# Kernel optimization log

Hardware: AMD Instinct MI355X
Metric: run time of the kernel (lower is better)

## Reference

```python
import jax, jax.numpy as jnp
from jax import lax
import numpy as np

POOL = 9   # nms_threshold*2 + 1
PAD = 4    # POOL // 2


def setup_inputs() -> dict:
    key = jax.random.key(0)
    x = jax.random.normal(key, (4, 256, 200, 320), dtype=jnp.float32)
    return {"x": x}


def reference(x):
    # x: [B, C, H, W]
    depth_wise_max = jnp.max(x, axis=1, keepdims=True)          # [B,1,H,W]
    is_depth_wise_max = x == depth_wise_max                      # [B,C,H,W] bool
    # 9x9 local max pool, stride 1, pad 4 (torch pads with -inf for max_pool2d)
    local_max = lax.reduce_window(
        x, -jnp.inf, lax.max,
        window_dimensions=(1, 1, POOL, POOL),
        window_strides=(1, 1, 1, 1),
        padding=[(0, 0), (0, 0), (PAD, PAD), (PAD, PAD)],
    )
    is_local_max = x == local_max
    prob = jnp.where(is_depth_wise_max & is_local_max, x, jnp.zeros((), x.dtype)).sum(axis=1)  # [B,H,W]
    return prob
```

## Files before the change

kernel.cpp:

```cpp
#include <hip/hip_runtime.h>
#include <math.h>

#define B_   4
#define C_   256
#define H_   200
#define W_   320
#define HW   (H_ * W_)
#define BHW  (B_ * HW)

#define TH   50
#define TW   64
#define PR   58
#define PCW  72
#define PSTRIDE 76
#define HSTRIDE 68
#define CS   16
#define CPG  (C_ / CS)

static_assert(TH * 4 == H_, "H tiling");
static_assert(TW * 5 == W_, "W tiling");

__device__ __forceinline__ void win9(const float v[16], float w[8]) {
  float m1[15];
#pragma unroll
  for (int i = 0; i < 15; ++i) m1[i] = fmaxf(v[i], v[i + 1]);
  float m2[13];
#pragma unroll
  for (int i = 0; i < 13; ++i) m2[i] = fmaxf(m1[i], m1[i + 2]);
  float m4[9];
#pragma unroll
  for (int i = 0; i < 9; ++i)  m4[i] = fmaxf(m2[i], m2[i + 4]);
#pragma unroll
  for (int i = 0; i < 8; ++i)  w[i] = fmaxf(m4[i], v[i + 8]);
}

__global__ __launch_bounds__(256) void hdm_main(const float* __restrict__ x,
                                                float* __restrict__ wsM,
                                                float* __restrict__ wsP) {
  __shared__ float patch[PR * PSTRIDE];
  __shared__ float hmax[PR * HSTRIDE];

  const int tile = blockIdx.x;
  const int b    = blockIdx.y;
  const int cg   = blockIdx.z;
  const int th   = tile / 5, tw = tile % 5;
  const int h0 = th * TH, w0 = tw * TW;
  const int tid = (int)threadIdx.x;

  const int rvA   = tid;
  const int rsegA = rvA >> 6, cwA = rvA & 63;
  const int r0A   = rsegA * 8;
  const int rvB   = tid + 256;
  const bool actB = rvB < 7 * 64;
  const int rsegB = rvB >> 6, cwB = rvB & 63;
  const int r0B   = rsegB * 8;
  const int kvB   = (rsegB == 6) ? 2 : 8;

  float accM0[8], accP0[8], accM1[8], accP1[8];
#pragma unroll
  for (int i = 0; i < 8; ++i) {
    accM0[i] = -INFINITY; accP0[i] = 0.f;
    accM1[i] = -INFINITY; accP1[i] = 0.f;
  }

  for (int cc = 0; cc < CPG; ++cc) {
    const int c = cg * CPG + cc;
    const float* xp = x + (size_t)(b * C_ + c) * HW;

    for (int q = tid; q < PR * 18; q += 256) {
      const int pr = q / 18, c4 = q % 18;
      const int pc = c4 * 4;
      const int gh = h0 - 4 + pr;
      const int gw = w0 - 4 + pc;
      float4 v;
      if (gh < 0 || gh >= H_) {
        v.x = v.y = v.z = v.w = -INFINITY;
      } else if (gw >= 0 && gw + 3 < W_) {
        v = *reinterpret_cast<const float4*>(xp + (size_t)gh * W_ + gw);
      } else {
        const float* row = xp + (size_t)gh * W_;
        v.x = (gw + 0 >= 0 && gw + 0 < W_) ? row[gw + 0] : -INFINITY;
        v.y = (gw + 1 >= 0 && gw + 1 < W_) ? row[gw + 1] : -INFINITY;
        v.z = (gw + 2 >= 0 && gw + 2 < W_) ? row[gw + 2] : -INFINITY;
        v.w = (gw + 3 >= 0 && gw + 3 < W_) ? row[gw + 3] : -INFINITY;
      }
      *reinterpret_cast<float4*>(&patch[pr * PSTRIDE + pc]) = v;
    }
    __syncthreads();

    for (int rr = tid; rr < PR * 8; rr += 256) {
      const int r = rr >> 3, seg = rr & 7;
      const float* prow = &patch[r * PSTRIDE + seg * 8];
      const float4 a0 = *reinterpret_cast<const float4*>(prow + 0);
      const float4 a1 = *reinterpret_cast<const float4*>(prow + 4);
      const float4 a2 = *reinterpret_cast<const float4*>(prow + 8);
      const float4 a3 = *reinterpret_cast<const float4*>(prow + 12);
      const float v[16] = {a0.x, a0.y, a0.z, a0.w, a1.x, a1.y, a1.z, a1.w,
                           a2.x, a2.y, a2.z, a2.w, a3.x, a3.y, a3.z, a3.w};
      float w[8];
      win9(v, w);
      float* hrow = &hmax[r * HSTRIDE + seg * 8];
      *reinterpret_cast<float4*>(hrow + 0) = make_float4(w[0], w[1], w[2], w[3]);
      *reinterpret_cast<float4*>(hrow + 4) = make_float4(w[4], w[5], w[6], w[7]);
    }
    __syncthreads();

    {
      float hv[16];
#pragma unroll
      for (int i = 0; i < 16; ++i) hv[i] = hmax[(r0A + i) * HSTRIDE + cwA];
      float w9v[8];
      win9(hv, w9v);
#pragma unroll
      for (int i = 0; i < 8; ++i) {
        const float xc  = patch[(r0A + 4 + i) * PSTRIDE + (cwA + 4)];
        const float add = (xc == w9v[i]) ? xc : 0.f;
        const bool  gt  = xc > accM0[i];
        const bool  eq  = xc == accM0[i];
        accP0[i] = gt ? add : (accP0[i] + (eq ? add : 0.f));
        accM0[i] = gt ? xc : accM0[i];
      }
    }
    if (actB) {
      float hv[16];
#pragma unroll
      for (int i = 0; i < 16; ++i) {
        int r = r0B + i;
        r = (r < PR) ? r : (PR - 1);
        hv[i] = hmax[r * HSTRIDE + cwB];
      }
      float w9v[8];
      win9(hv, w9v);
#pragma unroll
      for (int i = 0; i < 8; ++i) {
        if (i < kvB) {
          const float xc  = patch[(r0B + 4 + i) * PSTRIDE + (cwB + 4)];
          const float add = (xc == w9v[i]) ? xc : 0.f;
          const bool  gt  = xc > accM1[i];
          const bool  eq  = xc == accM1[i];
          accP1[i] = gt ? add : (accP1[i] + (eq ? add : 0.f));
          accM1[i] = gt ? xc : accM1[i];
        }
      }
    }
    __syncthreads();
  }

  const size_t obase = (size_t)cg * BHW + (size_t)b * HW;
#pragma unroll
  for (int i = 0; i < 8; ++i) {
    const int h = h0 + r0A + i, w = w0 + cwA;
    const size_t idx = obase + (size_t)h * W_ + w;
    wsM[idx] = accM0[i];
    wsP[idx] = accP0[i];
  }
  if (actB) {
#pragma unroll
    for (int i = 0; i < 8; ++i) {
      if (i < kvB) {
        const int h = h0 + r0B + i, w = w0 + cwB;
        const size_t idx = obase + (size_t)h * W_ + w;
        wsM[idx] = accM1[i];
        wsP[idx] = accP1[i];
      }
    }
  }
}

__global__ __launch_bounds__(256) void hdm_combine(const float* __restrict__ wsM,
                                                   const float* __restrict__ wsP,
                                                   float* __restrict__ out) {
  const int px = blockIdx.x * 256 + (int)threadIdx.x;
  if (px >= BHW) return;
  float gm = -INFINITY, p = 0.f;
#pragma unroll
  for (int cs = 0; cs < CS; ++cs) {
    const float m = wsM[(size_t)cs * BHW + px];
    const float q = wsP[(size_t)cs * BHW + px];
    const bool gt = m > gm;
    const bool eq = m == gm;
    p  = gt ? q : (p + (eq ? q : 0.f));
    gm = gt ? m : gm;
  }
  out[px] = p;
}

extern "C" void kernel_launch(void* const* d_in, const int* in_sizes, int n_in,
                              void* d_out, int out_size, void* d_ws, size_t ws_size,
                              hipStream_t stream) {
  const float* x = (const float*)d_in[0];
  float* wsM = (float*)d_ws;
  float* wsP = wsM + (size_t)CS * BHW;
  float* out = (float*)d_out;

  hipLaunchKernelGGL(hdm_main, dim3(20, B_, CS), dim3(256), 0, stream, x, wsM, wsP);
  hipLaunchKernelGGL(hdm_combine, dim3((BHW + 255) / 256), dim3(256), 0, stream,
                     wsM, wsP, out);
}
```

Before: 433.4 us.

## Load patch rows into registers with prefetch, compute horizontal max before LDS

Each thread now loads its 16-wide row segment straight from global memory into registers, computes the horizontal 9-wide max there, and writes only the hmax row and the center values to shared memory. This removes the staging patch buffer and one pass through shared memory. The next channel's loads are issued before the barrier so global latency overlaps with the current channel's compute. The window max now uses max3 chains, and launch bounds request 4 blocks per SM. In exchange, register pressure rises from the prefetched float4s, and edge handling now relies on clamped loads plus register shifts.

```diff
diff --git a/kernel.cpp b/kernel.cpp
--- a/kernel.cpp
+++ b/kernel.cpp
@@ -11,50 +11,69 @@
 #define TH   50
 #define TW   64
 #define PR   58
-#define PCW  72
-#define PSTRIDE 76
-#define HSTRIDE 68
+#define HSTR 68
+#define XSTR 68
 #define CS   16
 #define CPG  (C_ / CS)
 
 static_assert(TH * 4 == H_, "H tiling");
 static_assert(TW * 5 == W_, "W tiling");
 
-__device__ __forceinline__ void win9(const float v[16], float w[8]) {
-  float m1[15];
-#pragma unroll
-  for (int i = 0; i < 15; ++i) m1[i] = fmaxf(v[i], v[i + 1]);
-  float m2[13];
-#pragma unroll
-  for (int i = 0; i < 13; ++i) m2[i] = fmaxf(m1[i], m1[i + 2]);
-  float m4[9];
-#pragma unroll
-  for (int i = 0; i < 9; ++i)  m4[i] = fmaxf(m2[i], m2[i + 4]);
-#pragma unroll
-  for (int i = 0; i < 8; ++i)  w[i] = fmaxf(m4[i], v[i + 8]);
-}
-
-__global__ __launch_bounds__(256) void hdm_main(const float* __restrict__ x,
-                                                float* __restrict__ wsM,
-                                                float* __restrict__ wsP) {
-  __shared__ float patch[PR * PSTRIDE];
-  __shared__ float hmax[PR * HSTRIDE];
+__device__ __forceinline__ float max3f(float a, float b, float c) {
+  return fmaxf(fmaxf(a, b), c);
+}
+
+__device__ __forceinline__ void win9m3(const float v[16], float w[8]) {
+  float m3[14];
+#pragma unroll
+  for (int i = 0; i < 14; ++i) m3[i] = max3f(v[i], v[i + 1], v[i + 2]);
+#pragma unroll
+  for (int i = 0; i < 8; ++i)  w[i] = max3f(m3[i], m3[i + 3], m3[i + 6]);
+}
+
+#define LD4(p, o) (*reinterpret_cast<const float4*>((p) + (o)))
+
+__global__ __launch_bounds__(256, 4) void hdm_main(const float* __restrict__ x,
+                                                   float* __restrict__ wsM,
+                                                   float* __restrict__ wsP) {
+  __shared__ float hmax[PR * HSTR];
+  __shared__ float xcen[TH * XSTR];
 
   const int tile = blockIdx.x;
   const int b    = blockIdx.y;
   const int cg   = blockIdx.z;
-  const int th   = tile / 5, tw = tile % 5;
+  const int th = tile / 5, tw = tile % 5;
   const int h0 = th * TH, w0 = tw * TW;
   const int tid = (int)threadIdx.x;
 
-  const int rvA   = tid;
-  const int rsegA = rvA >> 6, cwA = rvA & 63;
-  const int r0A   = rsegA * 8;
-  const int rvB   = tid + 256;
-  const bool actB = rvB < 7 * 64;
-  const int rsegB = rvB >> 6, cwB = rvB & 63;
-  const int r0B   = rsegB * 8;
-  const int kvB   = (rsegB == 6) ? 2 : 8;
+  const float* xg = x + (size_t)(b * C_ + cg * CPG) * HW;
+
+  const int  rA   = tid >> 3, sA = tid & 7;
+  const int  ghA  = h0 - 4 + rA;
+  const bool rokA = (ghA >= 0) && (ghA < H_);
+  const int  gwA  = w0 - 4 + sA * 8;
+  const bool lftA = (gwA < 0), rgtA = (gwA + 16 > W_);
+  const int  gwcA = lftA ? 0 : (rgtA ? (W_ - 16) : gwA);
+  const int  ghcA = min(max(ghA, 0), H_ - 1);
+  const float* pA = xg + (size_t)ghcA * W_ + gwcA;
+  const bool wxA  = rokA && (rA >= 4) && (rA <= 53);
+
+  const bool actB1 = tid < (PR * 8 - 256);
+  const int  qB   = tid + 256;
+  const int  rB   = qB >> 3, sB = qB & 7;
+  const int  ghB  = h0 - 4 + rB;
+  const bool rokB = (ghB >= 0) && (ghB < H_);
+  const int  gwB  = w0 - 4 + sB * 8;
+  const bool lftB = (gwB < 0), rgtB = (gwB + 16 > W_);
+  const int  gwcB = lftB ? 0 : (rgtB ? (W_ - 16) : gwB);
+  const int  ghcB = min(max(ghB, 0), H_ - 1);
+  const float* pB = xg + (size_t)ghcB * W_ + gwcB;
+  const bool wxB  = rokB && (rB >= 4) && (rB <= 53);
+
+  const int rs2A = tid >> 6, cw2 = tid & 63, r02A = rs2A * 8;
+  const bool actB2 = tid < 192;
+  const int rs2B = (tid + 256) >> 6, r02B = rs2B * 8;
+  const int kvB2 = (rs2B == 6) ? 2 : 8;
 
   float accM0[8], accP0[8], accM1[8], accP1[8];
 #pragma unroll
@@ -63,79 +82,135 @@
     accM1[i] = -INFINITY; accP1[i] = 0.f;
   }
 
+  float4 A0 = LD4(pA, 0), A1 = LD4(pA, 4), A2 = LD4(pA, 8), A3 = LD4(pA, 12);
+  float4 B0, B1, B2, B3;
+  if (actB1) { B0 = LD4(pB, 0); B1 = LD4(pB, 4); B2 = LD4(pB, 8); B3 = LD4(pB, 12); }
+  pA += HW; pB += HW;
+
   for (int cc = 0; cc < CPG; ++cc) {
-    const int c = cg * CPG + cc;
-    const float* xp = x + (size_t)(b * C_ + c) * HW;
-
-    for (int q = tid; q < PR * 18; q += 256) {
-      const int pr = q / 18, c4 = q % 18;
-      const int pc = c4 * 4;
-      const int gh = h0 - 4 + pr;
-      const int gw = w0 - 4 + pc;
-      float4 v;
-      if (gh < 0 || gh >= H_) {
-        v.x = v.y = v.z = v.w = -INFINITY;
-      } else if (gw >= 0 && gw + 3 < W_) {
-        v = *reinterpret_cast<const float4*>(xp + (size_t)gh * W_ + gw);
-      } else {
-        const float* row = xp + (size_t)gh * W_;
-        v.x = (gw + 0 >= 0 && gw + 0 < W_) ? row[gw + 0] : -INFINITY;
-        v.y = (gw + 1 >= 0 && gw + 1 < W_) ? row[gw + 1] : -INFINITY;
-        v.z = (gw + 2 >= 0 && gw + 2 < W_) ? row[gw + 2] : -INFINITY;
-        v.w = (gw + 3 >= 0 && gw + 3 < W_) ? row[gw + 3] : -INFINITY;
-      }
-      *reinterpret_cast<float4*>(&patch[pr * PSTRIDE + pc]) = v;
-    }
+    float wA[8];
+    float4 xAlo, xAhi;
+    {
+      const float t[16] = {A0.x, A0.y, A0.z, A0.w, A1.x, A1.y, A1.z, A1.w,
+                           A2.x, A2.y, A2.z, A2.w, A3.x, A3.y, A3.z, A3.w};
+      float v[16];
+      if (lftA) {
+#pragma unroll
+        for (int j = 0; j < 4;  ++j) v[j] = -INFINITY;
+#pragma unroll
+        for (int j = 4; j < 16; ++j) v[j] = t[j - 4];
+      } else if (rgtA) {
+#pragma unroll
+        for (int j = 0; j < 12; ++j) v[j] = t[j + 4];
+#pragma unroll
+        for (int j = 12; j < 16; ++j) v[j] = -INFINITY;
+      } else {
+#pragma unroll
+        for (int j = 0; j < 16; ++j) v[j] = t[j];
+      }
+      if (rokA) {
+        win9m3(v, wA);
+      } else {
+#pragma unroll
+        for (int i = 0; i < 8; ++i) wA[i] = -INFINITY;
+      }
+      xAlo = make_float4(v[4], v[5], v[6], v[7]);
+      xAhi = make_float4(v[8], v[9], v[10], v[11]);
+    }
+    float wB[8];
+    float4 xBlo, xBhi;
+    if (actB1) {
+      const float t[16] = {B0.x, B0.y, B0.z, B0.w, B1.x, B1.y, B1.z, B1.w,
+                           B2.x, B2.y, B2.z, B2.w, B3.x, B3.y, B3.z, B3.w};
+      float v[16];
+      if (lftB) {
+#pragma unroll
+        for (int j = 0; j < 4;  ++j) v[j] = -INFINITY;
+#pragma unroll
+        for (int j = 4; j < 16; ++j) v[j] = t[j - 4];
+      } else if (rgtB) {
+#pragma unroll
+        for (int j = 0; j < 12; ++j) v[j] = t[j + 4];
+#pragma unroll
+        for (int j = 12; j < 16; ++j) v[j] = -INFINITY;
+      } else {
+#pragma unroll
+        for (int j = 0; j < 16; ++j) v[j] = t[j];
+      }
+      if (rokB) {
+        win9m3(v, wB);
+      } else {
+#pragma unroll
+        for (int i = 0; i < 8; ++i) wB[i] = -INFINITY;
+      }
+      xBlo = make_float4(v[4], v[5], v[6], v[7]);
+      xBhi = make_float4(v[8], v[9], v[10], v[11]);
+    }
+
+    if (cc + 1 < CPG) {
+      A0 = LD4(pA, 0); A1 = LD4(pA, 4); A2 = LD4(pA, 8); A3 = LD4(pA, 12);
+      pA += HW;
+      if (actB1) {
+        B0 = LD4(pB, 0); B1 = LD4(pB, 4); B2 = LD4(pB, 8); B3 = LD4(pB, 12);
+        pB += HW;
+      }
+    }
+
     __syncthreads();
 
-    for (int rr = tid; rr < PR * 8; rr += 256) {
-      const int r = rr >> 3, seg = rr & 7;
-      const float* prow = &patch[r * PSTRIDE + seg * 8];
-      const float4 a0 = *reinterpret_cast<const float4*>(prow + 0);
-      const float4 a1 = *reinterpret_cast<const float4*>(prow + 4);
-      const float4 a2 = *reinterpret_cast<const float4*>(prow + 8);
-      const float4 a3 = *reinterpret_cast<const float4*>(prow + 12);
-      const float v[16] = {a0.x, a0.y, a0.z, a0.w, a1.x, a1.y, a1.z, a1.w,
-                           a2.x, a2.y, a2.z, a2.w, a3.x, a3.y, a3.z, a3.w};
-      float w[8];
-      win9(v, w);
-      float* hrow = &hmax[r * HSTRIDE + seg * 8];
-      *reinterpret_cast<float4*>(hrow + 0) = make_float4(w[0], w[1], w[2], w[3]);
-      *reinterpret_cast<float4*>(hrow + 4) = make_float4(w[4], w[5], w[6], w[7]);
-    }
+    {
+      float* hr = &hmax[rA * HSTR + sA * 8];
+      *reinterpret_cast<float4*>(hr + 0) = make_float4(wA[0], wA[1], wA[2], wA[3]);
+      *reinterpret_cast<float4*>(hr + 4) = make_float4(wA[4], wA[5], wA[6], wA[7]);
+      if (wxA) {
+        float* xr = &xcen[(rA - 4) * XSTR + sA * 8];
+        *reinterpret_cast<float4*>(xr + 0) = xAlo;
+        *reinterpret_cast<float4*>(xr + 4) = xAhi;
+      }
+      if (actB1) {
+        float* hrb = &hmax[rB * HSTR + sB * 8];
+        *reinterpret_cast<float4*>(hrb + 0) = make_float4(wB[0], wB[1], wB[2], wB[3]);
+        *reinterpret_cast<float4*>(hrb + 4) = make_float4(wB[4], wB[5], wB[6], wB[7]);
+        if (wxB) {
+          float* xrb = &xcen[(rB - 4) * XSTR + sB * 8];
+          *reinterpret_cast<float4*>(xrb + 0) = xBlo;
+          *reinterpret_cast<float4*>(xrb + 4) = xBhi;
+        }
+      }
+    }
+
     __syncthreads();
 
     {
       float hv[16];
 #pragma unroll
-      for (int i = 0; i < 16; ++i) hv[i] = hmax[(r0A + i) * HSTRIDE + cwA];
-      float w9v[8];
-      win9(hv, w9v);
+      for (int i = 0; i < 16; ++i) hv[i] = hmax[(r02A + i) * HSTR + cw2];
+      float w9[8];
+      win9m3(hv, w9);
 #pragma unroll
       for (int i = 0; i < 8; ++i) {
-        const float xc  = patch[(r0A + 4 + i) * PSTRIDE + (cwA + 4)];
-        const float add = (xc == w9v[i]) ? xc : 0.f;
+        const float xc  = xcen[(r02A + i) * XSTR + cw2];
+        const float add = (xc == w9[i]) ? xc : 0.f;
         const bool  gt  = xc > accM0[i];
         const bool  eq  = xc == accM0[i];
         accP0[i] = gt ? add : (accP0[i] + (eq ? add : 0.f));
         accM0[i] = gt ? xc : accM0[i];
       }
     }
-    if (actB) {
+    if (actB2) {
       float hv[16];
 #pragma unroll
       for (int i = 0; i < 16; ++i) {
-        int r = r0B + i;
-        r = (r < PR) ? r : (PR - 1);
-        hv[i] = hmax[r * HSTRIDE + cwB];
-      }
-      float w9v[8];
-      win9(hv, w9v);
+        const int r = min(r02B + i, PR - 1);
+        hv[i] = hmax[r * HSTR + cw2];
+      }
+      float w9[8];
+      win9m3(hv, w9);
 #pragma unroll
       for (int i = 0; i < 8; ++i) {
-        if (i < kvB) {
-          const float xc  = patch[(r0B + 4 + i) * PSTRIDE + (cwB + 4)];
-          const float add = (xc == w9v[i]) ? xc : 0.f;
+        if (i < kvB2) {
+          const float xc  = xcen[(r02B + i) * XSTR + cw2];
+          const float add = (xc == w9[i]) ? xc : 0.f;
           const bool  gt  = xc > accM1[i];
           const bool  eq  = xc == accM1[i];
           accP1[i] = gt ? add : (accP1[i] + (eq ? add : 0.f));
@@ -149,17 +224,15 @@
   const size_t obase = (size_t)cg * BHW + (size_t)b * HW;
 #pragma unroll
   for (int i = 0; i < 8; ++i) {
-    const int h = h0 + r0A + i, w = w0 + cwA;
-    const size_t idx = obase + (size_t)h * W_ + w;
+    const size_t idx = obase + (size_t)(h0 + r02A + i) * W_ + (w0 + cw2);
     wsM[idx] = accM0[i];
     wsP[idx] = accP0[i];
   }
-  if (actB) {
+  if (actB2) {
 #pragma unroll
     for (int i = 0; i < 8; ++i) {
-      if (i < kvB) {
-        const int h = h0 + r0B + i, w = w0 + cwB;
-        const size_t idx = obase + (size_t)h * W_ + w;
+      if (i < kvB2) {
+        const size_t idx = obase + (size_t)(h0 + r02B + i) * W_ + (w0 + cw2);
         wsM[idx] = accM1[i];
         wsP[idx] = accP1[i];
       }
```

Result: slower. 551.7 us (+27.3%).

## Load rows directly to registers, double-buffer LDS, and cut barriers per channel

Applied to the files above, without the earlier changes.

Each thread now loads its 16-wide row segment straight from global memory into registers and computes the horizontal 9-max in registers. This removes the raw patch staging in shared memory, and the next channel's loads are prefetched while the current one is processed. The hmax and centre buffers are double-buffered so each channel needs a single __syncthreads instead of three. The block grows to 512 threads with one output column-group per thread, and the window max uses max3 chains. Edge handling relies on shifting clamped loads, and register pressure from the prefetch may limit occupancy.

```diff
diff --git a/kernel.cpp b/kernel.cpp
--- a/kernel.cpp
+++ b/kernel.cpp
@@ -11,157 +11,143 @@
 #define TH   50
 #define TW   64
 #define PR   58
-#define PCW  72
-#define PSTRIDE 76
-#define HSTRIDE 68
+#define HSTR 68
+#define XSTR 68
 #define CS   16
 #define CPG  (C_ / CS)
+#define NT   512
+
+#define HBUF (PR * HSTR)
+#define XBUF (TH * XSTR)
 
 static_assert(TH * 4 == H_, "H tiling");
 static_assert(TW * 5 == W_, "W tiling");
 
-__device__ __forceinline__ void win9(const float v[16], float w[8]) {
-  float m1[15];
-#pragma unroll
-  for (int i = 0; i < 15; ++i) m1[i] = fmaxf(v[i], v[i + 1]);
-  float m2[13];
-#pragma unroll
-  for (int i = 0; i < 13; ++i) m2[i] = fmaxf(m1[i], m1[i + 2]);
-  float m4[9];
-#pragma unroll
-  for (int i = 0; i < 9; ++i)  m4[i] = fmaxf(m2[i], m2[i + 4]);
-#pragma unroll
-  for (int i = 0; i < 8; ++i)  w[i] = fmaxf(m4[i], v[i + 8]);
+__device__ __forceinline__ float max3f(float a, float b, float c) {
+  return fmaxf(fmaxf(a, b), c);
 }
 
-__global__ __launch_bounds__(256) void hdm_main(const float* __restrict__ x,
-                                                float* __restrict__ wsM,
-                                                float* __restrict__ wsP) {
-  __shared__ float patch[PR * PSTRIDE];
-  __shared__ float hmax[PR * HSTRIDE];
+__device__ __forceinline__ void win9m3(const float v[16], float w[8]) {
+  float m3[14];
+#pragma unroll
+  for (int i = 0; i < 14; ++i) m3[i] = max3f(v[i], v[i + 1], v[i + 2]);
+#pragma unroll
+  for (int i = 0; i < 8; ++i)  w[i] = max3f(m3[i], m3[i + 3], m3[i + 6]);
+}
+
+#define LD4(p, o) (*reinterpret_cast<const float4*>((p) + (o)))
+
+__global__ __launch_bounds__(NT, 4) void hdm_main(const float* __restrict__ x,
+                                                  float* __restrict__ wsM,
+                                                  float* __restrict__ wsP) {
+  __shared__ float hmax[2 * HBUF];
+  __shared__ float xcen[2 * XBUF];
 
   const int tile = blockIdx.x;
   const int b    = blockIdx.y;
   const int cg   = blockIdx.z;
-  const int th   = tile / 5, tw = tile % 5;
+  const int th = tile / 5, tw = tile % 5;
   const int h0 = th * TH, w0 = tw * TW;
   const int tid = (int)threadIdx.x;
 
-  const int rvA   = tid;
-  const int rsegA = rvA >> 6, cwA = rvA & 63;
-  const int r0A   = rsegA * 8;
-  const int rvB   = tid + 256;
-  const bool actB = rvB < 7 * 64;
-  const int rsegB = rvB >> 6, cwB = rvB & 63;
-  const int r0B   = rsegB * 8;
-  const int kvB   = (rsegB == 6) ? 2 : 8;
+  const float* xg = x + (size_t)(b * C_ + cg * CPG) * HW;
 
-  float accM0[8], accP0[8], accM1[8], accP1[8];
+  const bool act1 = tid < PR * 8;
+  const int  r1   = tid >> 3, s1 = tid & 7;
+  const int  gh   = h0 - 4 + r1;
+  const bool rok  = (gh >= 0) && (gh < H_);
+  const int  gw   = w0 - 4 + s1 * 8;
+  const bool lft  = (gw < 0), rgt = (gw + 16 > W_);
+  const int  gwc  = lft ? 0 : (rgt ? (W_ - 16) : gw);
+  const int  ghc  = min(max(gh, 0), H_ - 1);
+  const float* p1 = xg + (size_t)ghc * W_ + gwc;
+  const bool wx   = (r1 >= 4) && (r1 <= 53);
+
+  const bool act2 = tid < 448;
+  const int  rs2  = tid >> 6, cw2 = tid & 63, r02 = rs2 * 8;
+  const int  kv   = (rs2 == 6) ? 2 : 8;
+
+  float accM[8], accP[8];
 #pragma unroll
-  for (int i = 0; i < 8; ++i) {
-    accM0[i] = -INFINITY; accP0[i] = 0.f;
-    accM1[i] = -INFINITY; accP1[i] = 0.f;
+  for (int i = 0; i < 8; ++i) { accM[i] = -INFINITY; accP[i] = 0.f; }
+
+  float4 A0, A1, A2, A3;
+  if (act1) {
+    A0 = LD4(p1, 0); A1 = LD4(p1, 4); A2 = LD4(p1, 8); A3 = LD4(p1, 12);
+    p1 += HW;
   }
 
   for (int cc = 0; cc < CPG; ++cc) {
-    const int c = cg * CPG + cc;
-    const float* xp = x + (size_t)(b * C_ + c) * HW;
+    float wH[8];
+    float4 xlo, xhi;
+    {
+      const float tt[16] = {A0.x, A0.y, A0.z, A0.w, A1.x, A1.y, A1.z, A1.w,
+                            A2.x, A2.y, A2.z, A2.w, A3.x, A3.y, A3.z, A3.w};
+      float v[16];
+#pragma unroll
+      for (int j = 0; j < 16; ++j) {
+        const float va = (j >= 4)  ? tt[j - 4] : -INFINITY;
+        const float vb = (j < 12)  ? tt[j + 4] : -INFINITY;
+        v[j] = lft ? va : (rgt ? vb : tt[j]);
+      }
+      win9m3(v, wH);
+#pragma unroll
+      for (int i = 0; i < 8; ++i) wH[i] = rok ? wH[i] : -INFINITY;
+      xlo = make_float4(v[4], v[5], v[6], v[7]);
+      xhi = make_float4(v[8], v[9], v[10], v[11]);
+    }
 
-    for (int q = tid; q < PR * 18; q += 256) {
-      const int pr = q / 18, c4 = q % 18;
-      const int pc = c4 * 4;
-      const int gh = h0 - 4 + pr;
-      const int gw = w0 - 4 + pc;
-      float4 v;
-      if (gh < 0 || gh >= H_) {
-        v.x = v.y = v.z = v.w = -INFINITY;
-      } else if (gw >= 0 && gw + 3 < W_) {
-        v = *reinterpret_cast<const float4*>(xp + (size_t)gh * W_ + gw);
-      } else {
-        const float* row = xp + (size_t)gh * W_;
-        v.x = (gw + 0 >= 0 && gw + 0 < W_) ? row[gw + 0] : -INFINITY;
-        v.y = (gw + 1 >= 0 && gw + 1 < W_) ? row[gw + 1] : -INFINITY;
-        v.z = (gw + 2 >= 0 && gw + 2 < W_) ? row[gw + 2] : -INFINITY;
-        v.w = (gw + 3 >= 0 && gw + 3 < W_) ? row[gw + 3] : -INFINITY;
+    if (act1 && (cc + 1 < CPG)) {
+      A0 = LD4(p1, 0); A1 = LD4(p1, 4); A2 = LD4(p1, 8); A3 = LD4(p1, 12);
+      p1 += HW;
+    }
+
+    float* hb = &hmax[(cc & 1) * HBUF];
+    float* xb = &xcen[(cc & 1) * XBUF];
+    if (act1) {
+      float* hr = hb + r1 * HSTR + s1 * 8;
+      *reinterpret_cast<float4*>(hr + 0) = make_float4(wH[0], wH[1], wH[2], wH[3]);
+      *reinterpret_cast<float4*>(hr + 4) = make_float4(wH[4], wH[5], wH[6], wH[7]);
+      if (wx) {
+        float* xr = xb + (r1 - 4) * XSTR + s1 * 8;
+        *reinterpret_cast<float4*>(xr + 0) = xlo;
+        *reinterpret_cast<float4*>(xr + 4) = xhi;
       }
-      *reinterpret_cast<float4*>(&patch[pr * PSTRIDE + pc]) = v;
     }
+
     __syncthreads();
 
-    for (int rr = tid; rr < PR * 8; rr += 256) {
-      const int r = rr >> 3, seg = rr & 7;
-      const float* prow = &patch[r * PSTRIDE + seg * 8];
-      const float4 a0 = *reinterpret_cast<const float4*>(prow + 0);
-      const float4 a1 = *reinterpret_cast<const float4*>(prow + 4);
-      const float4 a2 = *reinterpret_cast<const float4*>(prow + 8);
-      const float4 a3 = *reinterpret_cast<const float4*>(prow + 12);
-      const float v[16] = {a0.x, a0.y, a0.z, a0.w, a1.x, a1.y, a1.z, a1.w,
-                           a2.x, a2.y, a2.z, a2.w, a3.x, a3.y, a3.z, a3.w};
-      float w[8];
-      win9(v, w);
-      float* hrow = &hmax[r * HSTRIDE + seg * 8];
-      *reinterpret_cast<float4*>(hrow + 0) = make_float4(w[0], w[1], w[2], w[3]);
-      *reinterpret_cast<float4*>(hrow + 4) = make_float4(w[4], w[5], w[6], w[7]);
-    }
-    __syncthreads();
-
-    {
-      float hv[16];
-#pragma unroll
-      for (int i = 0; i < 16; ++i) hv[i] = hmax[(r0A + i) * HSTRIDE + cwA];
-      float w9v[8];
-      win9(hv, w9v);
-#pragma unroll
-      for (int i = 0; i < 8; ++i) {
-        const float xc  = patch[(r0A + 4 + i) * PSTRIDE + (cwA + 4)];
-        const float add = (xc == w9v[i]) ? xc : 0.f;
-        const bool  gt  = xc > accM0[i];
-        const bool  eq  = xc == accM0[i];
-        accP0[i] = gt ? add : (accP0[i] + (eq ? add : 0.f));
-        accM0[i] = gt ? xc : accM0[i];
-      }
-    }
-    if (actB) {
+    if (act2) {
       float hv[16];
 #pragma unroll
       for (int i = 0; i < 16; ++i) {
-        int r = r0B + i;
-        r = (r < PR) ? r : (PR - 1);
-        hv[i] = hmax[r * HSTRIDE + cwB];
+        const int r = min(r02 + i, PR - 1);
+        hv[i] = hb[r * HSTR + cw2];
       }
-      float w9v[8];
-      win9(hv, w9v);
+      float w9[8];
+      win9m3(hv, w9);
 #pragma unroll
       for (int i = 0; i < 8; ++i) {
-        if (i < kvB) {
-          const float xc  = patch[(r0B + 4 + i) * PSTRIDE + (cwB + 4)];
-          const float add = (xc == w9v[i]) ? xc : 0.f;
-          const bool  gt  = xc > accM1[i];
-          const bool  eq  = xc == accM1[i];
-          accP1[i] = gt ? add : (accP1[i] + (eq ? add : 0.f));
-          accM1[i] = gt ? xc : accM1[i];
+        if (i < kv) {
+          const float xc  = xb[(r02 + i) * XSTR + cw2];
+          const float add = (xc == w9[i]) ? xc : 0.f;
+          const bool  gt  = xc > accM[i];
+          const bool  eq  = xc == accM[i];
+          accP[i] = gt ? add : (accP[i] + (eq ? add : 0.f));
+          accM[i] = gt ? xc : accM[i];
         }
       }
     }
-    __syncthreads();
   }
 
-  const size_t obase = (size_t)cg * BHW + (size_t)b * HW;
-#pragma unroll
-  for (int i = 0; i < 8; ++i) {
-    const int h = h0 + r0A + i, w = w0 + cwA;
-    const size_t idx = obase + (size_t)h * W_ + w;
-    wsM[idx] = accM0[i];
-    wsP[idx] = accP0[i];
-  }
-  if (actB) {
+  if (act2) {
+    const size_t obase = (size_t)cg * BHW + (size_t)b * HW;
 #pragma unroll
     for (int i = 0; i < 8; ++i) {
-      if (i < kvB) {
-        const int h = h0 + r0B + i, w = w0 + cwB;
-        const size_t idx = obase + (size_t)h * W_ + w;
-        wsM[idx] = accM1[i];
-        wsP[idx] = accP1[i];
+      if (i < kv) {
+        const size_t idx = obase + (size_t)(h0 + r02 + i) * W_ + (w0 + cw2);
+        wsM[idx] = accM[i];
+        wsP[idx] = accP[i];
       }
     }
   }
@@ -193,7 +179,7 @@
   float* wsP = wsM + (size_t)CS * BHW;
   float* out = (float*)d_out;
 
-  hipLaunchKernelGGL(hdm_main, dim3(20, B_, CS), dim3(256), 0, stream, x, wsM, wsP);
+  hipLaunchKernelGGL(hdm_main, dim3(20, B_, CS), dim3(NT), 0, stream, x, wsM, wsP);
   hipLaunchKernelGGL(hdm_combine, dim3((BHW + 255) / 256), dim3(256), 0, stream,
                      wsM, wsP, out);
 }
```

Result: faster. 368.4 us (-15.0%).
